# Kernel optimization log

Measured on AMD Instinct MI355X. Metric: run time of the kernel, lower is better.

The kernel has to match this reference:

```python
import jax, jax.numpy as jnp
import numpy as np

B, T = 2048, 512
H1, H2, H3 = 100, 60, 30


def _glorot(key, shape, fan):
    bound = 1.0 / np.sqrt(fan)
    return jax.random.uniform(key, shape, jnp.float32, -bound, bound)


def setup_inputs() -> dict:
    key = jax.random.key(0)
    ks = jax.random.split(key, 17)
    inp = {"x": jax.random.normal(ks[0], (B, T, 2), jnp.float32)}
    # layer 1: input 2 -> hidden 100
    inp["W_ih1"] = _glorot(ks[1], (H1, 2), H1)
    inp["W_hh1"] = _glorot(ks[2], (H1, H1), H1)
    inp["b_ih1"] = _glorot(ks[3], (H1,), H1)
    inp["b_hh1"] = _glorot(ks[4], (H1,), H1)
    # layer 2: 100 -> 60
    inp["W_ih2"] = _glorot(ks[5], (H2, H1), H2)
    inp["W_hh2"] = _glorot(ks[6], (H2, H2), H2)
    inp["b_ih2"] = _glorot(ks[7], (H2,), H2)
    inp["b_hh2"] = _glorot(ks[8], (H2,), H2)
    # layer 3: 60 -> 30
    inp["W_ih3"] = _glorot(ks[9], (H3, H2), H3)
    inp["W_hh3"] = _glorot(ks[10], (H3, H3), H3)
    inp["b_ih3"] = _glorot(ks[11], (H3,), H3)
    inp["b_hh3"] = _glorot(ks[12], (H3,), H3)
    # heads
    inp["W_o1"] = _glorot(ks[13], (10, H3), 10)
    inp["b_o1"] = _glorot(ks[14], (10,), 10)
    inp["W_o2"] = _glorot(ks[15], (2, 10), 2)
    inp["b_o2"] = _glorot(ks[16], (2,), 2)
    return inp


def rnn_layer(x, W_ih, W_hh, b_ih, b_hh):
    # x: [B, T, in]; precompute the time-parallel input projection once
    xp = jnp.einsum("bti,hi->bth", x, W_ih) + (b_ih + b_hh)  # [B, T, H]
    h0 = jnp.zeros((x.shape[0], W_hh.shape[0]), x.dtype)

    def step(h, xt):  # xt: [B, H]
        h = jnp.tanh(xt + h @ W_hh.T)
        return h, h

    _, ys = jax.lax.scan(step, h0, jnp.swapaxes(xp, 0, 1))  # [T, B, H]
    return jnp.swapaxes(ys, 0, 1)  # [B, T, H]


def reference(x, W_ih1, W_hh1, b_ih1, b_hh1, W_ih2, W_hh2, b_ih2, b_hh2,
              W_ih3, W_hh3, b_ih3, b_hh3, W_o1, b_o1, W_o2, b_o2):
    h = rnn_layer(x, W_ih1, W_hh1, b_ih1, b_hh1)
    h = rnn_layer(h, W_ih2, W_hh2, b_ih2, b_hh2)
    h = rnn_layer(h, W_ih3, W_hh3, b_ih3, b_hh3)
    o = jnp.einsum("bth,oh->bto", h, W_o1) + b_o1
    return jnp.einsum("bto,po->btp", o, W_o2) + b_o2  # [B, T, 2]
```

## Files before the change

kernel.cpp:

```cpp
#include <hip/hip_runtime.h>

typedef _Float16 v8hf __attribute__((ext_vector_type(8)));
typedef float    v4f  __attribute__((ext_vector_type(4)));

#define MFMA16(a, b, c) __builtin_amdgcn_mfma_f32_16x16x32_f16((a), (b), (c), 0, 0, 0)

#define TT 512
#define BT 16
#define NTH 512

__shared__ __align__(16) _Float16 h1b[2][BT][136];
__shared__ __align__(16) _Float16 h2b[2][BT][72];
__shared__ __align__(16) _Float16 h3b[2][BT][40];
__shared__ __align__(16) _Float16 xst[TT][2 * BT];
__shared__ __align__(16) float    oring[BT][128][2];

__device__ __forceinline__ v4f tanh4(v4f r) {
    const float KS = 2.8853900817779268f;
    const float CL = 13.8498724f;
    float z0 = fminf(CL, fmaxf(-CL, r[0] * KS));
    float z1 = fminf(CL, fmaxf(-CL, r[1] * KS));
    float z2 = fminf(CL, fmaxf(-CL, r[2] * KS));
    float z3 = fminf(CL, fmaxf(-CL, r[3] * KS));
    float a0 = __builtin_amdgcn_exp2f(z0) + 1.f;
    float a1 = __builtin_amdgcn_exp2f(z1) + 1.f;
    float a2 = __builtin_amdgcn_exp2f(z2) + 1.f;
    float a3 = __builtin_amdgcn_exp2f(z3) + 1.f;
    float P = a0 * a1, Q = a2 * a3;
    float R = __builtin_amdgcn_rcpf(P * Q);
    float iP = Q * R, iQ = P * R;
    v4f t;
    t[0] = 1.f - 2.f * (a1 * iP);
    t[1] = 1.f - 2.f * (a0 * iP);
    t[2] = 1.f - 2.f * (a3 * iQ);
    t[3] = 1.f - 2.f * (a2 * iQ);
    return t;
}

__global__ __launch_bounds__(NTH)
void rnn3_w8(const float* __restrict__ xg,
             const float* __restrict__ Wih1, const float* __restrict__ Whh1,
             const float* __restrict__ bih1, const float* __restrict__ bhh1,
             const float* __restrict__ Wih2, const float* __restrict__ Whh2,
             const float* __restrict__ bih2, const float* __restrict__ bhh2,
             const float* __restrict__ Wih3, const float* __restrict__ Whh3,
             const float* __restrict__ bih3, const float* __restrict__ bhh3,
             const float* __restrict__ Wo1,  const float* __restrict__ bo1,
             const float* __restrict__ Wo2,  const float* __restrict__ bo2,
             float* __restrict__ outg)
{
    const int tid   = threadIdx.x;
    const int lane  = tid & 63;
    const int wid   = tid >> 6;
    const int col   = lane & 15;
    const int g     = lane >> 4;
    const int bbase = blockIdx.x * BT;

    {
        _Float16* z1 = &h1b[0][0][0];
        for (int i = tid; i < 2 * BT * 136; i += NTH) z1[i] = (_Float16)0.f;
        _Float16* z2 = &h2b[0][0][0];
        for (int i = tid; i < 2 * BT * 72; i += NTH) z2[i] = (_Float16)0.f;
        _Float16* z3 = &h3b[0][0][0];
        for (int i = tid; i < 2 * BT * 40; i += NTH) z3[i] = (_Float16)0.f;
        for (int i = tid; i < BT * TT * 2; i += NTH) {
            float v = xg[(size_t)bbase * (TT * 2) + i];
            int b = i >> 10, r = i & 1023, t = r >> 1, c = r & 1;
            xst[t][b * 2 + c] = (_Float16)v;
        }
    }

    v8hf F[9];
    #pragma unroll
    for (int i = 0; i < 9; ++i) F[i] = (v8hf)(_Float16)0.f;
    float bb0 = 0.f, bb1 = 0.f;

    auto ldW = [&](const float* W, int rows, int cols, int j, int kt) -> v8hf {
        v8hf r;
        #pragma unroll
        for (int e = 0; e < 8; ++e) {
            const int k = kt * 32 + g * 8 + e;
            float v = (j < rows && k < cols) ? W[j * cols + k] : 0.f;
            r[e] = (_Float16)v;
        }
        return r;
    };
    auto ldW1 = [&](int j, int kt) -> v8hf {
        v8hf r;
        #pragma unroll
        for (int e = 0; e < 8; ++e) {
            const int k = kt * 32 + g * 8 + e;
            float v = 0.f;
            if (j < 100) {
                if (k < 100)       v = Whh1[j * 100 + k];
                else if (k == 112) v = Wih1[j * 2];
                else if (k == 113) v = Wih1[j * 2 + 1];
            }
            r[e] = (_Float16)v;
        }
        return r;
    };
    auto bL1 = [&](int j) -> float { return (j < 100) ? bih1[j] + bhh1[j] : 0.f; };
    auto bL2 = [&](int j) -> float { return (j < 60) ? bih2[j] + bhh2[j] : 0.f; };
    auto bL3 = [&](int j) -> float { return (j < 30) ? bih3[j] + bhh3[j] : 0.f; };

    if (wid < 3) {
        const int ja = 32 * wid + col, jb = ja + 16;
        #pragma unroll
        for (int kt = 0; kt < 4; ++kt) { F[0 + kt] = ldW1(ja, kt); F[4 + kt] = ldW1(jb, kt); }
        bb0 = bL1(ja); bb1 = bL1(jb);
    } else if (wid == 3) {
        #pragma unroll
        for (int kt = 0; kt < 4; ++kt) F[kt] = ldW1(col + 96, kt);
        bb0 = bL1(col + 96);
    } else if (wid < 6) {
        const int j = col + 16 * (wid - 4);
        #pragma unroll
        for (int kt = 0; kt < 4; ++kt) F[kt] = ldW(Wih2, 60, 100, j, kt);
        F[4] = ldW(Whh2, 60, 60, j, 0);  F[5] = ldW(Whh2, 60, 60, j, 1);
        F[6] = ldW(Wih3, 30, 60, j, 0);  F[7] = ldW(Wih3, 30, 60, j, 1);
        F[8] = ldW(Whh3, 30, 30, j, 0);
        bb0 = bL2(j); bb1 = bL3(j);
    } else if (wid == 6) {
        const int j = col + 32;
        #pragma unroll
        for (int kt = 0; kt < 4; ++kt) F[kt] = ldW(Wih2, 60, 100, j, kt);
        F[4] = ldW(Whh2, 60, 60, j, 0);  F[5] = ldW(Whh2, 60, 60, j, 1);
        bb0 = bL2(j);
    } else {
        const int j = col + 48;
        #pragma unroll
        for (int kt = 0; kt < 4; ++kt) F[kt] = ldW(Wih2, 60, 100, j, kt);
        F[4] = ldW(Whh2, 60, 60, j, 0);  F[5] = ldW(Whh2, 60, 60, j, 1);
        bb0 = bL2(j);
        #pragma unroll
        for (int e = 0; e < 8; ++e) {
            const int k = g * 8 + e;
            float v = 0.f;
            if (col < 2 && k < 30) {
                #pragma unroll
                for (int u = 0; u < 10; ++u) v += Wo2[col * 10 + u] * Wo1[u * 30 + k];
            }
            F[6][e] = (_Float16)v;
        }
        if (col < 2) {
            float bv = bo2[col];
            #pragma unroll
            for (int u = 0; u < 10; ++u) bv += Wo2[col * 10 + u] * bo1[u];
            bb1 = bv;
        }
    }

    __syncthreads();
    if (tid < BT)
        *(unsigned*)&h1b[0][tid][112] = *(const unsigned*)&xst[0][tid * 2];
    __syncthreads();

#define WR_H1(r, jw) { _Pragma("unroll") for (int i = 0; i < 4; ++i) h1b[wp][4*g+i][jw] = (_Float16)(r)[i]; }
#define WR_H2(r, jw) { _Pragma("unroll") for (int i = 0; i < 4; ++i) h2b[rp][4*g+i][jw] = (_Float16)(r)[i]; }
#define WR_H3(r, jw) { _Pragma("unroll") for (int i = 0; i < 4; ++i) h3b[wp][4*g+i][jw] = (_Float16)(r)[i]; }

#define L1_TILE(f0, f1, f2, f3, bias, jw) { \
    v4f p = {bias, bias, bias, bias}, q = {0.f, 0.f, 0.f, 0.f}; \
    p = MFMA16(A0, f0, p); q = MFMA16(A1, f1, q); \
    p = MFMA16(A2, f2, p); q = MFMA16(A3, f3, q); \
    v4f r = tanh4(p + q); WR_H1(r, jw); }

#define L2_TILE(f0, f1, f2, f3, f4, f5, bias, jw) { \
    v4f p = {bias, bias, bias, bias}, q = {0.f, 0.f, 0.f, 0.f}; \
    p = MFMA16(A0, f0, p); q = MFMA16(A1, f1, q); \
    p = MFMA16(A2, f2, p); q = MFMA16(A3, f3, q); \
    p = MFMA16(B0, f4, p); q = MFMA16(B1, f5, q); \
    v4f r = tanh4(p + q); WR_H2(r, jw); }

#define L3_TILE(f0, f1, f2, bias, jw) { \
    v4f p = {bias, bias, bias, bias}, q = {0.f, 0.f, 0.f, 0.f}; \
    p = MFMA16(B0, f0, p); q = MFMA16(B1, f1, q); \
    p = MFMA16(C0, f2, p); \
    v4f r = tanh4(p + q); WR_H3(r, jw); }

    for (int s = 0; s < TT + 4; ++s) {
        const int rp = s & 1, wp = rp ^ 1;
        const _Float16* h1p = &h1b[rp][col][g * 8];
        const _Float16* h2p = &h2b[wp][col][g * 8];
        const _Float16* h3p = &h3b[rp][col][g * 8];

        if (wid < 3) {
            v8hf A0 = *(const v8hf*)(h1p);      v8hf A1 = *(const v8hf*)(h1p + 32);
            v8hf A2 = *(const v8hf*)(h1p + 64); v8hf A3 = *(const v8hf*)(h1p + 96);
            if (s < TT) {
                const int j0 = 32 * wid + col;
                L1_TILE(F[0], F[1], F[2], F[3], bb0, j0);
                L1_TILE(F[4], F[5], F[6], F[7], bb1, j0 + 16);
            }
        } else if (wid == 3) {
            if (lane < BT && s < TT - 1)
                *(unsigned*)&h1b[wp][lane][112] = *(const unsigned*)&xst[s + 1][2 * lane];
            v8hf A0 = *(const v8hf*)(h1p);      v8hf A1 = *(const v8hf*)(h1p + 32);
            v8hf A2 = *(const v8hf*)(h1p + 64); v8hf A3 = *(const v8hf*)(h1p + 96);
            if (s < TT)
                L1_TILE(F[0], F[1], F[2], F[3], bb0, col + 96);
            if (s >= 67 && ((s - 4) & 63) == 63) {
                const int tbase = s - 67;
                const int base4 = (tbase & 127) >> 1;
                const float4* ring4 = (const float4*)&oring[0][0][0];
                #pragma unroll
                for (int jj = 0; jj < 8; ++jj) {
                    const int f = lane + 64 * jj;
                    const int b = f >> 5, k = f & 31;
                    float4 v = ring4[b * 64 + base4 + k];
                    *(float4*)(outg + ((size_t)(bbase + b) * TT + tbase) * 2 + 4 * k) = v;
                }
            }
        } else if (wid < 6) {
            v8hf A0 = *(const v8hf*)(h1p);      v8hf A1 = *(const v8hf*)(h1p + 32);
            v8hf A2 = *(const v8hf*)(h1p + 64); v8hf A3 = *(const v8hf*)(h1p + 96);
            v8hf B0 = *(const v8hf*)(h2p);      v8hf B1 = *(const v8hf*)(h2p + 32);
            v8hf C0 = *(const v8hf*)(h3p);
            const int j0 = col + 16 * (wid - 4);
            if (s >= 1 && s <= TT)
                L2_TILE(F[0], F[1], F[2], F[3], F[4], F[5], bb0, j0);
            if (s >= 2 && s <= TT + 1)
                L3_TILE(F[6], F[7], F[8], bb1, j0);
        } else if (wid == 6) {
            v8hf A0 = *(const v8hf*)(h1p);      v8hf A1 = *(const v8hf*)(h1p + 32);
            v8hf A2 = *(const v8hf*)(h1p + 64); v8hf A3 = *(const v8hf*)(h1p + 96);
            v8hf B0 = *(const v8hf*)(h2p);      v8hf B1 = *(const v8hf*)(h2p + 32);
            if (s >= 1 && s <= TT)
                L2_TILE(F[0], F[1], F[2], F[3], F[4], F[5], bb0, col + 32);
        } else {
            v8hf A0 = *(const v8hf*)(h1p);      v8hf A1 = *(const v8hf*)(h1p + 32);
            v8hf A2 = *(const v8hf*)(h1p + 64); v8hf A3 = *(const v8hf*)(h1p + 96);
            v8hf B0 = *(const v8hf*)(h2p);      v8hf B1 = *(const v8hf*)(h2p + 32);
            v8hf C0 = *(const v8hf*)(h3p);
            if (s >= 1 && s <= TT)
                L2_TILE(F[0], F[1], F[2], F[3], F[4], F[5], bb0, col + 48);
            if (s >= 3 && s <= TT + 2) {
                const int t = s - 3;
                v4f o = {bb1, bb1, bb1, bb1};
                o = MFMA16(C0, F[6], o);
                if (col < 2) {
                    #pragma unroll
                    for (int i = 0; i < 4; ++i) oring[4 * g + i][t & 127][col] = o[i];
                }
            }
        }
        __syncthreads();
    }
}

extern "C" void kernel_launch(void* const* d_in, const int* in_sizes, int n_in,
                              void* d_out, int out_size, void* d_ws, size_t ws_size,
                              hipStream_t stream) {
    (void)in_sizes; (void)n_in; (void)d_ws; (void)ws_size; (void)out_size;
    const float* x     = (const float*)d_in[0];
    const float* W_ih1 = (const float*)d_in[1];
    const float* W_hh1 = (const float*)d_in[2];
    const float* b_ih1 = (const float*)d_in[3];
    const float* b_hh1 = (const float*)d_in[4];
    const float* W_ih2 = (const float*)d_in[5];
    const float* W_hh2 = (const float*)d_in[6];
    const float* b_ih2 = (const float*)d_in[7];
    const float* b_hh2 = (const float*)d_in[8];
    const float* W_ih3 = (const float*)d_in[9];
    const float* W_hh3 = (const float*)d_in[10];
    const float* b_ih3 = (const float*)d_in[11];
    const float* b_hh3 = (const float*)d_in[12];
    const float* W_o1  = (const float*)d_in[13];
    const float* b_o1  = (const float*)d_in[14];
    const float* W_o2  = (const float*)d_in[15];
    const float* b_o2  = (const float*)d_in[16];
    float* out = (float*)d_out;

    rnn3_w8<<<2048 / BT, NTH, 0, stream>>>(
        x, W_ih1, W_hh1, b_ih1, b_hh1,
        W_ih2, W_hh2, b_ih2, b_hh2,
        W_ih3, W_hh3, b_ih3, b_hh3,
        W_o1, b_o1, W_o2, b_o2, out);
}
```

Before: 322.6 us.

## Rebalance warp roles: co-locate layer-2 with layer-1 waves, dedicate output waves

Reassigns work across the 8 waves so that waves 0-3 compute layer 1 and layer 2 tiles, sharing the same loaded h1 fragments. Waves 4-5 now handle only layer 3, wave 6 handles the fused output head, and wave 7 only drains the output ring to global memory. Shared memory becomes one byte-addressed arena whose ping-pong offsets are toggled by XOR instead of recomputing indices. The clamp is also changed to fmed3. The aim is to balance per-wave MFMA and tanh work along the per-step critical path. The risk is heavier register pressure in waves 0-3, and waves 0-2 now carry the most work per step.

```diff
diff --git a/kernel.cpp b/kernel.cpp
--- a/kernel.cpp
+++ b/kernel.cpp
@@ -9,19 +9,21 @@
 #define BT 16
 #define NTH 512
 
-__shared__ __align__(16) _Float16 h1b[2][BT][136];
-__shared__ __align__(16) _Float16 h2b[2][BT][72];
-__shared__ __align__(16) _Float16 h3b[2][BT][40];
-__shared__ __align__(16) _Float16 xst[TT][2 * BT];
-__shared__ __align__(16) float    oring[BT][128][2];
+#define PBLK  8192u
+#define H2OFF 4352u
+#define H3OFF 6656u
+#define XSTO  16384u
+#define RINGO 49152u
+
+__shared__ __align__(64) char SM[57344];
 
 __device__ __forceinline__ v4f tanh4(v4f r) {
     const float KS = 2.8853900817779268f;
     const float CL = 13.8498724f;
-    float z0 = fminf(CL, fmaxf(-CL, r[0] * KS));
-    float z1 = fminf(CL, fmaxf(-CL, r[1] * KS));
-    float z2 = fminf(CL, fmaxf(-CL, r[2] * KS));
-    float z3 = fminf(CL, fmaxf(-CL, r[3] * KS));
+    float z0 = __builtin_amdgcn_fmed3f(r[0] * KS, -CL, CL);
+    float z1 = __builtin_amdgcn_fmed3f(r[1] * KS, -CL, CL);
+    float z2 = __builtin_amdgcn_fmed3f(r[2] * KS, -CL, CL);
+    float z3 = __builtin_amdgcn_fmed3f(r[3] * KS, -CL, CL);
     float a0 = __builtin_amdgcn_exp2f(z0) + 1.f;
     float a1 = __builtin_amdgcn_exp2f(z1) + 1.f;
     float a2 = __builtin_amdgcn_exp2f(z2) + 1.f;
@@ -38,7 +40,7 @@
 }
 
 __global__ __launch_bounds__(NTH)
-void rnn3_w8(const float* __restrict__ xg,
+void rnn3_hl(const float* __restrict__ xg,
              const float* __restrict__ Wih1, const float* __restrict__ Whh1,
              const float* __restrict__ bih1, const float* __restrict__ bhh1,
              const float* __restrict__ Wih2, const float* __restrict__ Whh2,
@@ -57,23 +59,20 @@
     const int bbase = blockIdx.x * BT;
 
     {
-        _Float16* z1 = &h1b[0][0][0];
-        for (int i = tid; i < 2 * BT * 136; i += NTH) z1[i] = (_Float16)0.f;
-        _Float16* z2 = &h2b[0][0][0];
-        for (int i = tid; i < 2 * BT * 72; i += NTH) z2[i] = (_Float16)0.f;
-        _Float16* z3 = &h3b[0][0][0];
-        for (int i = tid; i < 2 * BT * 40; i += NTH) z3[i] = (_Float16)0.f;
+        float4 z = {0.f, 0.f, 0.f, 0.f};
+        float4* p4 = (float4*)SM;
+        for (int i = tid; i < 1024; i += NTH) p4[i] = z;
         for (int i = tid; i < BT * TT * 2; i += NTH) {
             float v = xg[(size_t)bbase * (TT * 2) + i];
             int b = i >> 10, r = i & 1023, t = r >> 1, c = r & 1;
-            xst[t][b * 2 + c] = (_Float16)v;
+            *(_Float16*)(SM + XSTO + (unsigned)t * 64u + (unsigned)b * 4u + (unsigned)c * 2u) = (_Float16)v;
         }
     }
 
-    v8hf F[9];
+    v8hf F[14];
     #pragma unroll
-    for (int i = 0; i < 9; ++i) F[i] = (v8hf)(_Float16)0.f;
-    float bb0 = 0.f, bb1 = 0.f;
+    for (int i = 0; i < 14; ++i) F[i] = (v8hf)(_Float16)0.f;
+    float bb0 = 0.f, bb1 = 0.f, bb2 = 0.f;
 
     auto ldW = [&](const float* W, int rows, int cols, int j, int kt) -> v8hf {
         v8hf r;
@@ -104,35 +103,39 @@
     auto bL2 = [&](int j) -> float { return (j < 60) ? bih2[j] + bhh2[j] : 0.f; };
     auto bL3 = [&](int j) -> float { return (j < 30) ? bih3[j] + bhh3[j] : 0.f; };
 
-    if (wid < 3) {
-        const int ja = 32 * wid + col, jb = ja + 16;
-        #pragma unroll
-        for (int kt = 0; kt < 4; ++kt) { F[0 + kt] = ldW1(ja, kt); F[4 + kt] = ldW1(jb, kt); }
-        bb0 = bL1(ja); bb1 = bL1(jb);
-    } else if (wid == 3) {
-        #pragma unroll
-        for (int kt = 0; kt < 4; ++kt) F[kt] = ldW1(col + 96, kt);
-        bb0 = bL1(col + 96);
+    unsigned oA = 0, oB = 0, oC = 0, oW1 = 0, oW2 = 0, oW3 = 0, oXw = 0, oRw = 0;
+
+    if (wid < 4) {
+        const int jA = 16 * wid + col;
+        #pragma unroll
+        for (int kt = 0; kt < 4; ++kt) {
+            F[0 + kt] = ldW1(jA, kt);
+            F[8 + kt] = ldW(Wih2, 60, 100, jA, kt);
+        }
+        F[12] = ldW(Whh2, 60, 60, jA, 0);
+        F[13] = ldW(Whh2, 60, 60, jA, 1);
+        bb0 = bL1(jA); bb2 = bL2(jA);
+        if (wid < 3) {
+            const int jB = jA + 64;
+            #pragma unroll
+            for (int kt = 0; kt < 4; ++kt) F[4 + kt] = ldW1(jB, kt);
+            bb1 = bL1(jB);
+        }
+        oA  = (unsigned)col * 272u + (unsigned)g * 16u;
+        oB  = PBLK + H2OFF + (unsigned)col * 144u + (unsigned)g * 16u;
+        oW1 = PBLK + (unsigned)(4 * g) * 272u + (unsigned)jA * 2u;
+        oW2 = H2OFF + (unsigned)(4 * g) * 144u + (unsigned)jA * 2u;
+        oXw = PBLK + (unsigned)lane * 272u + 224u;
     } else if (wid < 6) {
-        const int j = col + 16 * (wid - 4);
-        #pragma unroll
-        for (int kt = 0; kt < 4; ++kt) F[kt] = ldW(Wih2, 60, 100, j, kt);
-        F[4] = ldW(Whh2, 60, 60, j, 0);  F[5] = ldW(Whh2, 60, 60, j, 1);
-        F[6] = ldW(Wih3, 30, 60, j, 0);  F[7] = ldW(Wih3, 30, 60, j, 1);
-        F[8] = ldW(Whh3, 30, 30, j, 0);
-        bb0 = bL2(j); bb1 = bL3(j);
+        const int j3 = 16 * (wid - 4) + col;
+        F[0] = ldW(Wih3, 30, 60, j3, 0);
+        F[1] = ldW(Wih3, 30, 60, j3, 1);
+        F[2] = ldW(Whh3, 30, 30, j3, 0);
+        bb0 = bL3(j3);
+        oB  = PBLK + H2OFF + (unsigned)col * 144u + (unsigned)g * 16u;
+        oC  = H3OFF + (unsigned)col * 80u + (unsigned)g * 16u;
+        oW3 = PBLK + H3OFF + (unsigned)(4 * g) * 80u + (unsigned)j3 * 2u;
     } else if (wid == 6) {
-        const int j = col + 32;
-        #pragma unroll
-        for (int kt = 0; kt < 4; ++kt) F[kt] = ldW(Wih2, 60, 100, j, kt);
-        F[4] = ldW(Whh2, 60, 60, j, 0);  F[5] = ldW(Whh2, 60, 60, j, 1);
-        bb0 = bL2(j);
-    } else {
-        const int j = col + 48;
-        #pragma unroll
-        for (int kt = 0; kt < 4; ++kt) F[kt] = ldW(Wih2, 60, 100, j, kt);
-        F[4] = ldW(Whh2, 60, 60, j, 0);  F[5] = ldW(Whh2, 60, 60, j, 1);
-        bb0 = bL2(j);
         #pragma unroll
         for (int e = 0; e < 8; ++e) {
             const int k = g * 8 + e;
@@ -141,107 +144,111 @@
                 #pragma unroll
                 for (int u = 0; u < 10; ++u) v += Wo2[col * 10 + u] * Wo1[u * 30 + k];
             }
-            F[6][e] = (_Float16)v;
+            F[0][e] = (_Float16)v;
         }
         if (col < 2) {
             float bv = bo2[col];
             #pragma unroll
             for (int u = 0; u < 10; ++u) bv += Wo2[col * 10 + u] * bo1[u];
-            bb1 = bv;
-        }
+            bb0 = bv;
+        }
+        oC  = H3OFF + (unsigned)col * 80u + (unsigned)g * 16u;
+        oRw = RINGO + (unsigned)(4 * g) * 512u + (unsigned)col * 4u;
     }
 
     __syncthreads();
     if (tid < BT)
-        *(unsigned*)&h1b[0][tid][112] = *(const unsigned*)&xst[0][tid * 2];
+        *(unsigned*)(SM + (unsigned)tid * 272u + 224u) =
+            *(const unsigned*)(SM + XSTO + (unsigned)tid * 4u);
     __syncthreads();
 
-#define WR_H1(r, jw) { _Pragma("unroll") for (int i = 0; i < 4; ++i) h1b[wp][4*g+i][jw] = (_Float16)(r)[i]; }
-#define WR_H2(r, jw) { _Pragma("unroll") for (int i = 0; i < 4; ++i) h2b[rp][4*g+i][jw] = (_Float16)(r)[i]; }
-#define WR_H3(r, jw) { _Pragma("unroll") for (int i = 0; i < 4; ++i) h3b[wp][4*g+i][jw] = (_Float16)(r)[i]; }
-
-#define L1_TILE(f0, f1, f2, f3, bias, jw) { \
-    v4f p = {bias, bias, bias, bias}, q = {0.f, 0.f, 0.f, 0.f}; \
-    p = MFMA16(A0, f0, p); q = MFMA16(A1, f1, q); \
-    p = MFMA16(A2, f2, p); q = MFMA16(A3, f3, q); \
-    v4f r = tanh4(p + q); WR_H1(r, jw); }
-
-#define L2_TILE(f0, f1, f2, f3, f4, f5, bias, jw) { \
-    v4f p = {bias, bias, bias, bias}, q = {0.f, 0.f, 0.f, 0.f}; \
-    p = MFMA16(A0, f0, p); q = MFMA16(A1, f1, q); \
-    p = MFMA16(A2, f2, p); q = MFMA16(A3, f3, q); \
-    p = MFMA16(B0, f4, p); q = MFMA16(B1, f5, q); \
-    v4f r = tanh4(p + q); WR_H2(r, jw); }
-
-#define L3_TILE(f0, f1, f2, bias, jw) { \
-    v4f p = {bias, bias, bias, bias}, q = {0.f, 0.f, 0.f, 0.f}; \
-    p = MFMA16(B0, f0, p); q = MFMA16(B1, f1, q); \
-    p = MFMA16(C0, f2, p); \
-    v4f r = tanh4(p + q); WR_H3(r, jw); }
+#define ST_H1(r, EX) { \
+    *(_Float16*)(SM + oW1 + (EX) + 0u)   = (_Float16)(r)[0]; \
+    *(_Float16*)(SM + oW1 + (EX) + 272u) = (_Float16)(r)[1]; \
+    *(_Float16*)(SM + oW1 + (EX) + 544u) = (_Float16)(r)[2]; \
+    *(_Float16*)(SM + oW1 + (EX) + 816u) = (_Float16)(r)[3]; }
+#define ST_H2(r) { \
+    *(_Float16*)(SM + oW2 + 0u)   = (_Float16)(r)[0]; \
+    *(_Float16*)(SM + oW2 + 144u) = (_Float16)(r)[1]; \
+    *(_Float16*)(SM + oW2 + 288u) = (_Float16)(r)[2]; \
+    *(_Float16*)(SM + oW2 + 432u) = (_Float16)(r)[3]; }
+#define ST_H3(r) { \
+    *(_Float16*)(SM + oW3 + 0u)   = (_Float16)(r)[0]; \
+    *(_Float16*)(SM + oW3 + 80u)  = (_Float16)(r)[1]; \
+    *(_Float16*)(SM + oW3 + 160u) = (_Float16)(r)[2]; \
+    *(_Float16*)(SM + oW3 + 240u) = (_Float16)(r)[3]; }
 
     for (int s = 0; s < TT + 4; ++s) {
-        const int rp = s & 1, wp = rp ^ 1;
-        const _Float16* h1p = &h1b[rp][col][g * 8];
-        const _Float16* h2p = &h2b[wp][col][g * 8];
-        const _Float16* h3p = &h3b[rp][col][g * 8];
-
-        if (wid < 3) {
-            v8hf A0 = *(const v8hf*)(h1p);      v8hf A1 = *(const v8hf*)(h1p + 32);
-            v8hf A2 = *(const v8hf*)(h1p + 64); v8hf A3 = *(const v8hf*)(h1p + 96);
-            if (s < TT) {
-                const int j0 = 32 * wid + col;
-                L1_TILE(F[0], F[1], F[2], F[3], bb0, j0);
-                L1_TILE(F[4], F[5], F[6], F[7], bb1, j0 + 16);
-            }
-        } else if (wid == 3) {
-            if (lane < BT && s < TT - 1)
-                *(unsigned*)&h1b[wp][lane][112] = *(const unsigned*)&xst[s + 1][2 * lane];
-            v8hf A0 = *(const v8hf*)(h1p);      v8hf A1 = *(const v8hf*)(h1p + 32);
-            v8hf A2 = *(const v8hf*)(h1p + 64); v8hf A3 = *(const v8hf*)(h1p + 96);
-            if (s < TT)
-                L1_TILE(F[0], F[1], F[2], F[3], bb0, col + 96);
-            if (s >= 67 && ((s - 4) & 63) == 63) {
-                const int tbase = s - 67;
-                const int base4 = (tbase & 127) >> 1;
-                const float4* ring4 = (const float4*)&oring[0][0][0];
+        if (wid < 4) {
+            if (wid == 3 && lane < BT && s < TT - 1) {
+                unsigned xv = *(const unsigned*)(SM + XSTO + (unsigned)(s + 1) * 64u + (unsigned)lane * 4u);
+                *(unsigned*)(SM + oXw) = xv;
+            }
+            if (s <= TT) {
+                v8hf A0 = *(const v8hf*)(SM + oA);
+                v8hf A1 = *(const v8hf*)(SM + oA + 64u);
+                v8hf A2 = *(const v8hf*)(SM + oA + 128u);
+                v8hf A3 = *(const v8hf*)(SM + oA + 192u);
+                v8hf B0 = *(const v8hf*)(SM + oB);
+                v8hf B1 = *(const v8hf*)(SM + oB + 64u);
+                if (s < TT) {
+                    {
+                        v4f p = {bb0, bb0, bb0, bb0}, q = {0.f, 0.f, 0.f, 0.f};
+                        p = MFMA16(A0, F[0], p); q = MFMA16(A1, F[1], q);
+                        p = MFMA16(A2, F[2], p); q = MFMA16(A3, F[3], q);
+                        v4f r = tanh4(p + q); ST_H1(r, 0u);
+                    }
+                    if (wid < 3) {
+                        v4f p = {bb1, bb1, bb1, bb1}, q = {0.f, 0.f, 0.f, 0.f};
+                        p = MFMA16(A0, F[4], p); q = MFMA16(A1, F[5], q);
+                        p = MFMA16(A2, F[6], p); q = MFMA16(A3, F[7], q);
+                        v4f r = tanh4(p + q); ST_H1(r, 128u);
+                    }
+                }
+                if (s >= 1) {
+                    v4f p = {bb2, bb2, bb2, bb2}, q = {0.f, 0.f, 0.f, 0.f};
+                    p = MFMA16(A0, F[8],  p); q = MFMA16(A1, F[9],  q);
+                    p = MFMA16(A2, F[10], p); q = MFMA16(A3, F[11], q);
+                    p = MFMA16(B0, F[12], p); q = MFMA16(B1, F[13], q);
+                    v4f r = tanh4(p + q); ST_H2(r);
+                }
+            }
+            oA ^= PBLK; oB ^= PBLK; oW1 ^= PBLK; oW2 ^= PBLK; oXw ^= PBLK;
+        } else if (wid < 6) {
+            if (s >= 2 && s <= TT + 1) {
+                v8hf B0 = *(const v8hf*)(SM + oB);
+                v8hf B1 = *(const v8hf*)(SM + oB + 64u);
+                v8hf C0 = *(const v8hf*)(SM + oC);
+                v4f p = {bb0, bb0, bb0, bb0}, q = {0.f, 0.f, 0.f, 0.f};
+                p = MFMA16(B0, F[0], p); q = MFMA16(B1, F[1], q);
+                p = MFMA16(C0, F[2], p);
+                v4f r = tanh4(p + q); ST_H3(r);
+            }
+            oB ^= PBLK; oC ^= PBLK; oW3 ^= PBLK;
+        } else if (wid == 6) {
+            if (s >= 3 && s <= TT + 2) {
+                v8hf C0 = *(const v8hf*)(SM + oC);
+                v4f o = {bb0, bb0, bb0, bb0};
+                o = MFMA16(C0, F[0], o);
+                const unsigned so = ((unsigned)(s - 3) & 63u) * 8u;
+                if (col < 2) {
+                    *(float*)(SM + oRw + so + 0u)    = o[0];
+                    *(float*)(SM + oRw + so + 512u)  = o[1];
+                    *(float*)(SM + oRw + so + 1024u) = o[2];
+                    *(float*)(SM + oRw + so + 1536u) = o[3];
+                }
+            }
+            oC ^= PBLK;
+        } else {
+            if (s >= 35 && ((s - 4) & 31) == 31) {
+                const int tbase = s - 35;
+                const unsigned rb = RINGO + (((unsigned)tbase & 63u) >> 1) * 16u;
                 #pragma unroll
-                for (int jj = 0; jj < 8; ++jj) {
+                for (int jj = 0; jj < 4; ++jj) {
                     const int f = lane + 64 * jj;
-                    const int b = f >> 5, k = f & 31;
-                    float4 v = ring4[b * 64 + base4 + k];
+                    const int b = f >> 4, k = f & 15;
+                    float4 v = *(const float4*)(SM + rb + (unsigned)b * 512u + (unsigned)k * 16u);
                     *(float4*)(outg + ((size_t)(bbase + b) * TT + tbase) * 2 + 4 * k) = v;
-                }
-            }
-        } else if (wid < 6) {
-            v8hf A0 = *(const v8hf*)(h1p);      v8hf A1 = *(const v8hf*)(h1p + 32);
-            v8hf A2 = *(const v8hf*)(h1p + 64); v8hf A3 = *(const v8hf*)(h1p + 96);
-            v8hf B0 = *(const v8hf*)(h2p);      v8hf B1 = *(const v8hf*)(h2p + 32);
-            v8hf C0 = *(const v8hf*)(h3p);
-            const int j0 = col + 16 * (wid - 4);
-            if (s >= 1 && s <= TT)
-                L2_TILE(F[0], F[1], F[2], F[3], F[4], F[5], bb0, j0);
-            if (s >= 2 && s <= TT + 1)
-                L3_TILE(F[6], F[7], F[8], bb1, j0);
-        } else if (wid == 6) {
-            v8hf A0 = *(const v8hf*)(h1p);      v8hf A1 = *(const v8hf*)(h1p + 32);
-            v8hf A2 = *(const v8hf*)(h1p + 64); v8hf A3 = *(const v8hf*)(h1p + 96);
-            v8hf B0 = *(const v8hf*)(h2p);      v8hf B1 = *(const v8hf*)(h2p + 32);
-            if (s >= 1 && s <= TT)
-                L2_TILE(F[0], F[1], F[2], F[3], F[4], F[5], bb0, col + 32);
-        } else {
-            v8hf A0 = *(const v8hf*)(h1p);      v8hf A1 = *(const v8hf*)(h1p + 32);
-            v8hf A2 = *(const v8hf*)(h1p + 64); v8hf A3 = *(const v8hf*)(h1p + 96);
-            v8hf B0 = *(const v8hf*)(h2p);      v8hf B1 = *(const v8hf*)(h2p + 32);
-            v8hf C0 = *(const v8hf*)(h3p);
-            if (s >= 1 && s <= TT)
-                L2_TILE(F[0], F[1], F[2], F[3], F[4], F[5], bb0, col + 48);
-            if (s >= 3 && s <= TT + 2) {
-                const int t = s - 3;
-                v4f o = {bb1, bb1, bb1, bb1};
-                o = MFMA16(C0, F[6], o);
-                if (col < 2) {
-                    #pragma unroll
-                    for (int i = 0; i < 4; ++i) oring[4 * g + i][t & 127][col] = o[i];
                 }
             }
         }
@@ -272,7 +279,7 @@
     const float* b_o2  = (const float*)d_in[16];
     float* out = (float*)d_out;
 
-    rnn3_w8<<<2048 / BT, NTH, 0, stream>>>(
+    rnn3_hl<<<2048 / BT, NTH, 0, stream>>>(
         x, W_ih1, W_hh1, b_ih1, b_hh1,
         W_ih2, W_hh2, b_ih2, b_hh2,
         W_ih3, W_hh3, b_ih3, b_hh3,
```

New measurement: 311.5 us. 3.4% less time.
